# Performance work log

Measured on AMD Instinct MI355X. Metric: run time of the kernel, lower is better.

The kernel has to match this reference:

```python
import jax, jax.numpy as jnp
import numpy as np

HIDDEN = 2048
NUM_HEADS = 16
NUM_KV_HEADS = 4
HEAD_DIM = HIDDEN // NUM_HEADS  # 128
ROPE_THETA = 1000000.0
B, S = 2, 2048


def setup_inputs() -> dict:
    key = jax.random.key(0)
    ks = jax.random.split(key, 10)
    sc = 0.02
    return {
        "hidden_states": jax.random.normal(ks[0], (B, S, HIDDEN), jnp.float32),
        "position_ids": jnp.broadcast_to(jnp.arange(S, dtype=jnp.int32), (B, S)),
        "Wq": jax.random.normal(ks[1], (HIDDEN, NUM_HEADS * HEAD_DIM), jnp.float32) * sc,
        "bq": jnp.zeros((NUM_HEADS * HEAD_DIM,), jnp.float32),
        "Wk": jax.random.normal(ks[2], (HIDDEN, NUM_KV_HEADS * HEAD_DIM), jnp.float32) * sc,
        "bk": jnp.zeros((NUM_KV_HEADS * HEAD_DIM,), jnp.float32),
        "Wv": jax.random.normal(ks[3], (HIDDEN, NUM_KV_HEADS * HEAD_DIM), jnp.float32) * sc,
        "bv": jnp.zeros((NUM_KV_HEADS * HEAD_DIM,), jnp.float32),
        "Wo": jax.random.normal(ks[4], (NUM_HEADS * HEAD_DIM, HIDDEN), jnp.float32) * sc,
        "bo": jnp.zeros((HIDDEN,), jnp.float32),
    }


def _rope_cos_sin(position_ids, dtype):
    # inv_freq: [head_dim/2]
    inv_freq = 1.0 / (ROPE_THETA ** (jnp.arange(0, HEAD_DIM, 2, dtype=jnp.float32) / HEAD_DIM))
    freqs = position_ids.astype(jnp.float32)[:, :, None] * inv_freq[None, None, :]  # [B,S,d/2]
    emb = jnp.concatenate([freqs, freqs], axis=-1)  # [B,S,d]
    return jnp.cos(emb).astype(dtype), jnp.sin(emb).astype(dtype)


def _rotate_half(x):
    h = x.shape[-1] // 2
    return jnp.concatenate([-x[..., h:], x[..., :h]], axis=-1)


def _attention(hidden_states, position_ids, Wq, bq, Wk, bk, Wv, bv, Wo, bo):
    bsz, q_len, _ = hidden_states.shape
    q = (hidden_states @ Wq + bq).reshape(bsz, q_len, NUM_HEADS, HEAD_DIM).transpose(0, 2, 1, 3)
    k = (hidden_states @ Wk + bk).reshape(bsz, q_len, NUM_KV_HEADS, HEAD_DIM).transpose(0, 2, 1, 3)
    v = (hidden_states @ Wv + bv).reshape(bsz, q_len, NUM_KV_HEADS, HEAD_DIM).transpose(0, 2, 1, 3)

    cos, sin = _rope_cos_sin(position_ids, hidden_states.dtype)
    cos = cos[:, None, :, :]  # [B,1,S,d]
    sin = sin[:, None, :, :]
    q = q * cos + _rotate_half(q) * sin
    k = k * cos + _rotate_half(k) * sin

    # repeat_kv (GQA): [B,kvh,S,d] -> [B,H,S,d]
    n_rep = NUM_HEADS // NUM_KV_HEADS
    k = jnp.repeat(k, n_rep, axis=1)
    v = jnp.repeat(v, n_rep, axis=1)

    scale = 1.0 / jnp.sqrt(jnp.array(HEAD_DIM, hidden_states.dtype))
    scores = jnp.einsum('bhqd,bhkd->bhqk', q, k) * scale  # [B,H,S,S]
    causal = jnp.tril(jnp.ones((q_len, q_len), bool))
    scores = jnp.where(causal[None, None], scores, jnp.finfo(scores.dtype).min)
    probs = jax.nn.softmax(scores.astype(jnp.float32), axis=-1).astype(hidden_states.dtype)
    attn = jnp.einsum('bhqk,bhkd->bhqd', probs, v)
    attn = attn.transpose(0, 2, 1, 3).reshape(bsz, q_len, HIDDEN)
    return attn @ Wo + bo


def reference(hidden_states, position_ids, Wq, bq, Wk, bk, Wv, bv, Wo, bo):
    return _attention(hidden_states, position_ids, Wq, bq, Wk, bk, Wv, bv, Wo, bo)
```

## Files before the change

### kernel.cpp

```cpp
#include <hip/hip_runtime.h>
#include <cmath>

#define HIDDEN 2048
#define NH 16
#define NKV 4
#define HD 128
#define SEQ 2048
#define BATCH 2

typedef unsigned short ushort_t;
typedef short bf16x8 __attribute__((ext_vector_type(8)));
typedef float f32x4 __attribute__((ext_vector_type(4)));
typedef ushort_t u16x4 __attribute__((ext_vector_type(4)));

__device__ __forceinline__ ushort_t f2bf(float f) {
    union { float f; unsigned int u; } v; v.f = f;
    unsigned int r = v.u + 0x7fffu + ((v.u >> 16) & 1u);
    return (ushort_t)(r >> 16);
}
__device__ __forceinline__ ushort_t f2bf_trunc(float f) {
    union { float f; unsigned int u; } v; v.f = f;
    return (ushort_t)(v.u >> 16);
}

__device__ __forceinline__ f32x4 mfma16(bf16x8 a, bf16x8 b, f32x4 c) {
    return __builtin_amdgcn_mfma_f32_16x16x32_bf16(a, b, c, 0, 0, 0);
}

__device__ __forceinline__ void load_lds16(const void* g, void* l) {
    __builtin_amdgcn_global_load_lds((const __attribute__((address_space(1))) unsigned int*)g,
                                     (__attribute__((address_space(3))) unsigned int*)l,
                                     16, 0, 0);
}


__global__ __launch_bounds__(256) void convert_x(const float* __restrict__ x,
                                                 ushort_t* __restrict__ xb, int n4) {
    int g = blockIdx.x * 256 + threadIdx.x;
    if (g >= n4) return;
    float4 v = ((const float4*)x)[g];
    u16x4 o;
    o[0] = f2bf(v.x); o[1] = f2bf(v.y); o[2] = f2bf(v.z); o[3] = f2bf(v.w);
    ((u16x4*)xb)[g] = o;
}

__global__ __launch_bounds__(256) void transpose_all(const float* __restrict__ Wq,
                                                     const float* __restrict__ Wk,
                                                     const float* __restrict__ Wv,
                                                     const float* __restrict__ Wo,
                                                     ushort_t* __restrict__ WqkvT,
                                                     ushort_t* __restrict__ WoT) {
    const int z = blockIdx.z;
    const float* W;
    ushort_t* WT;
    int N;
    if (z == 0)      { W = Wq; WT = WqkvT;                        N = 2048; }
    else if (z == 1) { W = Wk; WT = WqkvT + 2048ull * 2048;       N = 512;  }
    else if (z == 2) { W = Wv; WT = WqkvT + 2560ull * 2048;       N = 512;  }
    else             { W = Wo; WT = WoT;                          N = 2048; }
    const int K = 2048;
    const int n0 = blockIdx.x * 64, k0 = blockIdx.y * 64;
    if (n0 >= N) return;
    __shared__ ushort_t T[64][72];
    const int t = threadIdx.x;
    for (int idx = t; idx < 64 * 16; idx += 256) {
        int r = idx >> 4, c4 = (idx & 15) << 2;
        float4 v = *(const float4*)&W[(size_t)(k0 + r) * N + n0 + c4];
        T[r][c4 + 0] = f2bf(v.x); T[r][c4 + 1] = f2bf(v.y);
        T[r][c4 + 2] = f2bf(v.z); T[r][c4 + 3] = f2bf(v.w);
    }
    __syncthreads();
    for (int idx = t; idx < 64 * 16; idx += 256) {
        int n = idx >> 4, kg = (idx & 15) << 2;
        u16x4 o;
        o[0] = T[kg + 0][n]; o[1] = T[kg + 1][n];
        o[2] = T[kg + 2][n]; o[3] = T[kg + 3][n];
        *(u16x4*)&WT[(size_t)(n0 + n) * K + k0 + kg] = o;
    }
}

template <int MODE, int BK>
__global__ __launch_bounds__(256) void gemm_bt(const ushort_t* __restrict__ A,
                                               const ushort_t* __restrict__ Bt,
                                               const float* __restrict__ bias,
                                               const float* __restrict__ bias2,
                                               const float* __restrict__ bias3,
                                               void* __restrict__ out,
                                               void* __restrict__ out2,
                                               void* __restrict__ out3,
                                               int M, int N, int K,
                                               const int* __restrict__ posids) {
    constexpr int CH = BK / 32;
    __shared__ __align__(16) ushort_t As[2 * CH * 4096];
    __shared__ __align__(16) ushort_t Bs[2 * CH * 4096];
    const int tid = threadIdx.x;
    const int w = tid >> 6, lane = tid & 63, quad = lane >> 4, l16 = lane & 15;
    const int wr = w >> 1, wc = w & 1;
    const int m0 = blockIdx.y * 128, n0 = blockIdx.x * 128;

    f32x4 acc[4][4];
    for (int i = 0; i < 4; i++)
        for (int j = 0; j < 4; j++)
            for (int e = 0; e < 4; e++) acc[i][j][e] = 0.0f;

    const int rr = lane >> 2;
    const int gc8 = (((lane & 3) ^ ((lane >> 3) & 3)) << 3);
    const ushort_t* Ag = A + (size_t)(m0 + w * 32 + rr) * K + gc8;
    const ushort_t* Bg = Bt + (size_t)(n0 + w * 32 + rr) * K + gc8;
    ushort_t* Asw = As + w * 1024;
    ushort_t* Bsw = Bs + w * 1024;

    auto stage = [&](int bi, int k0) {
#pragma unroll
        for (int kc = 0; kc < CH; kc++) {
            const ushort_t* ag = Ag + k0 + kc * 32;
            const ushort_t* bg = Bg + k0 + kc * 32;
            ushort_t* la = Asw + (bi * CH + kc) * 4096;
            ushort_t* lb = Bsw + (bi * CH + kc) * 4096;
            load_lds16(ag, la);
            load_lds16(ag + (size_t)16 * K, la + 512);
            load_lds16(bg, lb);
            load_lds16(bg + (size_t)16 * K, lb + 512);
        }
    };

    const int nk = K / BK;
    const int rsw = ((l16 >> 1) & 3);
    stage(0, 0);
    __syncthreads();

    for (int ki = 0; ki < nk; ki++) {
        const int cur = ki & 1;
        if (ki + 1 < nk) stage(cur ^ 1, (ki + 1) * BK);
#pragma unroll
        for (int kc = 0; kc < CH; kc++) {
            const ushort_t* Ab = &As[(cur * CH + kc) * 4096];
            const ushort_t* Bb = &Bs[(cur * CH + kc) * 4096];
            bf16x8 af[4];
#pragma unroll
            for (int i = 0; i < 4; i++)
                af[i] = *(const bf16x8*)&Ab[(wr * 64 + i * 16 + l16) * 32 + ((quad ^ rsw) << 3)];
#pragma unroll
            for (int j = 0; j < 4; j++) {
                bf16x8 bf = *(const bf16x8*)&Bb[((wc + 2 * j) * 16 + l16) * 32 +
                                                ((quad ^ rsw) << 3)];
#pragma unroll
                for (int i = 0; i < 4; i++) acc[i][j] = mfma16(af[i], bf, acc[i][j]);
            }
        }
        __syncthreads();
    }

    if (MODE == 0) {
        float* O = (float*)out;
#pragma unroll
        for (int i = 0; i < 4; i++)
#pragma unroll
            for (int r = 0; r < 4; r++) {
                int row = m0 + wr * 64 + i * 16 + quad * 4 + r;
#pragma unroll
                for (int j = 0; j < 4; j++) {
                    int col = n0 + (wc + 2 * j) * 16 + l16;
                    O[(size_t)row * N + col] = acc[i][j][r] + bias[col];
                }
            }
    } else {
        if (n0 < 2048) {
            ushort_t* O = (ushort_t*)out;
            const int h = n0 >> 7;
            const float scale = 0.08838834764831845f;
            float fr[2];
#pragma unroll
            for (int p = 0; p < 2; p++)
                fr[p] = __expf(-0.21586735246819178f * (float)((wc + 2 * p) * 16 + l16));
#pragma unroll
            for (int i = 0; i < 4; i++)
#pragma unroll
                for (int r = 0; r < 4; r++) {
                    int row = m0 + wr * 64 + i * 16 + quad * 4 + r;
                    int b = row >> 11, s = row & (SEQ - 1);
                    float pos = (float)posids[row];
                    size_t obase = ((size_t)(b * NH + h) * SEQ + s) * HD;
#pragma unroll
                    for (int p = 0; p < 2; p++) {
                        int dl = (wc + 2 * p) * 16 + l16;
                        float x1 = acc[i][p][r] + bias[n0 + dl];
                        float x2 = acc[i][p + 2][r] + bias[n0 + dl + 64];
                        float sn, cs;
                        __sincosf(pos * fr[p], &sn, &cs);
                        O[obase + dl]      = f2bf((x1 * cs - x2 * sn) * scale);
                        O[obase + dl + 64] = f2bf((x2 * cs + x1 * sn) * scale);
                    }
                }
        } else if (n0 < 2560) {
            ushort_t* O = (ushort_t*)out2;
            const int n0k = n0 - 2048;
            const int h = n0k >> 7;
            float fr[2];
#pragma unroll
            for (int p = 0; p < 2; p++)
                fr[p] = __expf(-0.21586735246819178f * (float)((wc + 2 * p) * 16 + l16));
#pragma unroll
            for (int i = 0; i < 4; i++)
#pragma unroll
                for (int r = 0; r < 4; r++) {
                    int row = m0 + wr * 64 + i * 16 + quad * 4 + r;
                    int b = row >> 11, s = row & (SEQ - 1);
                    float pos = (float)posids[row];
                    size_t obase = ((size_t)(b * NKV + h) * SEQ + s) * HD;
#pragma unroll
                    for (int p = 0; p < 2; p++) {
                        int dl = (wc + 2 * p) * 16 + l16;
                        float x1 = acc[i][p][r] + bias2[n0k + dl];
                        float x2 = acc[i][p + 2][r] + bias2[n0k + dl + 64];
                        float sn, cs;
                        __sincosf(pos * fr[p], &sn, &cs);
                        O[obase + dl]      = f2bf(x1 * cs - x2 * sn);
                        O[obase + dl + 64] = f2bf(x2 * cs + x1 * sn);
                    }
                }
        } else {
            ushort_t* O = (ushort_t*)out3;
            const int n0v = n0 - 2560;
            const int h = n0v >> 7;
#pragma unroll
            for (int i = 0; i < 4; i++)
#pragma unroll
                for (int r = 0; r < 4; r++) {
                    int row = m0 + wr * 64 + i * 16 + quad * 4 + r;
                    int b = row >> 11, s = row & (SEQ - 1);
#pragma unroll
                    for (int j = 0; j < 4; j++) {
                        int d = (wc + 2 * j) * 16 + l16;
                        float v = acc[i][j][r] + bias3[n0v + d];
                        O[((size_t)(b * NKV + h) * HD + d) * SEQ + s] = f2bf(v);
                    }
                }
        }
    }
}

__global__ __launch_bounds__(256) void flash(const ushort_t* __restrict__ Qr,
                                             const ushort_t* __restrict__ Kr,
                                             const ushort_t* __restrict__ Vt,
                                             ushort_t* __restrict__ Attn) {
    __shared__ __align__(16) ushort_t Ksh[2 * 4 * 64 * 32];
    __shared__ __align__(16) ushort_t Vsh[2 * 2 * 128 * 32];
    __shared__ __align__(16) ushort_t Ps[4 * 16 * 72];
    const int tid = threadIdx.x;
    const int w = tid >> 6, lane = tid & 63, quad = lane >> 4, l16 = lane & 15;
    const int x = blockIdx.x, h = blockIdx.y, b = blockIdx.z;
    const int qt = b ? x : (gridDim.x - 1 - x);
    const int q0 = qt * 128;
    const int nkt = 2 * qt + 2;
    const int hkv = h >> 2;
    const ushort_t* Kg = Kr + ((size_t)(b * NKV + hkv) * SEQ) * HD;
    const ushort_t* Vg = Vt + ((size_t)(b * NKV + hkv) * HD) * SEQ;

    const int p = lane >> 2;
    const int gc8 = (((lane & 3) ^ ((lane >> 3) & 3)) << 3);
    const ushort_t* kst = Kg + (size_t)p * HD + w * 32 + gc8;
    const ushort_t* vst = Vg + (size_t)((w & 1) * 64 + p) * SEQ + (w >> 1) * 32 + gc8;
    ushort_t* ksl = Ksh + w * 2048;
    ushort_t* vsl = Vsh + (w >> 1) * 4096 + (w & 1) * 2048;

    auto stage = [&](int bi, int kv0) {
        const ushort_t* gk = kst + (size_t)kv0 * HD;
        ushort_t* lk = ksl + bi * 8192;
        load_lds16(gk, lk);
        load_lds16(gk + (size_t)16 * HD, lk + 512);
        load_lds16(gk + (size_t)32 * HD, lk + 1024);
        load_lds16(gk + (size_t)48 * HD, lk + 1536);
        const ushort_t* gv = vst + kv0;
        ushort_t* lv = vsl + bi * 8192;
        load_lds16(gv, lv);
        load_lds16(gv + (size_t)16 * SEQ, lv + 512);
        load_lds16(gv + (size_t)32 * SEQ, lv + 1024);
        load_lds16(gv + (size_t)48 * SEQ, lv + 1536);
    };

    bf16x8 aq[2][4];
#pragma unroll
    for (int st = 0; st < 2; st++) {
        const size_t qrow = ((size_t)(b * NH + h) * SEQ + q0 + st * 64 + w * 16 + l16) * HD;
#pragma unroll
        for (int kc = 0; kc < 4; kc++)
            aq[st][kc] = *(const bf16x8*)&Qr[qrow + kc * 32 + quad * 8];
    }

    f32x4 o[2][8];
#pragma unroll
    for (int st = 0; st < 2; st++)
#pragma unroll
        for (int j = 0; j < 8; j++)
#pragma unroll
            for (int e = 0; e < 4; e++) o[st][j][e] = 0.0f;
    f32x4 ls2[2];
#pragma unroll
    for (int st = 0; st < 2; st++)
        for (int e = 0; e < 4; e++) ls2[st][e] = 0.0f;
    bf16x8 ones;
#pragma unroll
    for (int e = 0; e < 8; e++) ones[e] = (short)0x3F80;

    ushort_t* Pw = &Ps[w * 16 * 72];
    const int rsw8 = ((l16 >> 1) & 3) << 3;

    stage(0, 0);
    __syncthreads();

    for (int kt = 0; kt < nkt; kt++) {
        const int kv0 = kt * 64;
        const int cur = kt & 1;
        if (kt + 1 < nkt) stage(cur ^ 1, kv0 + 64);

        const ushort_t* Kb = Ksh + cur * 8192;
        const ushort_t* Vb = Vsh + cur * 8192;

#pragma unroll
        for (int st = 0; st < 2; st++) {
            if (st == 0 && kt == 2 * qt + 1) continue;

            f32x4 sa[4];
#pragma unroll
            for (int nt = 0; nt < 4; nt++)
#pragma unroll
                for (int e = 0; e < 4; e++) sa[nt][e] = 0.0f;
#pragma unroll
            for (int kc = 0; kc < 4; kc++) {
#pragma unroll
                for (int nt = 0; nt < 4; nt++) {
                    bf16x8 bk = *(const bf16x8*)&Kb[kc * 2048 + nt * 512 + l16 * 32 +
                                                    ((quad * 8) ^ rsw8)];
                    sa[nt] = mfma16(aq[st][kc], bk, sa[nt]);
                }
            }

            if ((kt >> 1) == qt && (kt & 1) == st) {
#pragma unroll
                for (int nt = 0; nt < 4; nt++)
#pragma unroll
                    for (int r = 0; r < 4; r++) {
                        int kvg = kv0 + nt * 16 + l16;
                        int qg = q0 + st * 64 + w * 16 + quad * 4 + r;
                        if (kvg > qg) sa[nt][r] = -1e30f;
                    }
            }

#pragma unroll
            for (int nt = 0; nt < 4; nt++)
#pragma unroll
                for (int r = 0; r < 4; r++)
                    Pw[(quad * 4 + r) * 72 + nt * 16 + l16] = f2bf_trunc(__expf(sa[nt][r]));

#pragma unroll
            for (int kc = 0; kc < 2; kc++) {
                bf16x8 ap = *(const bf16x8*)&Pw[l16 * 72 + kc * 32 + quad * 8];
                ls2[st] = mfma16(ap, ones, ls2[st]);
#pragma unroll
                for (int j = 0; j < 8; j++) {
                    bf16x8 bv = *(const bf16x8*)&Vb[kc * 4096 + (j * 16 + l16) * 32 +
                                                    ((quad * 8) ^ rsw8)];
                    o[st][j] = mfma16(ap, bv, o[st][j]);
                }
            }
        }
        __syncthreads();
    }

#pragma unroll
    for (int st = 0; st < 2; st++)
#pragma unroll
        for (int r = 0; r < 4; r++) {
            float inv = 1.0f / ls2[st][r];
            int row = b * SEQ + q0 + st * 64 + w * 16 + quad * 4 + r;
            size_t obase = (size_t)row * HIDDEN + h * HD;
#pragma unroll
            for (int j = 0; j < 8; j++) Attn[obase + j * 16 + l16] = f2bf(o[st][j][r] * inv);
        }
}

extern "C" void kernel_launch(void* const* d_in, const int* in_sizes, int n_in,
                              void* d_out, int out_size, void* d_ws, size_t ws_size,
                              hipStream_t stream) {
    const float* hs = (const float*)d_in[0];
    const int* posids = (const int*)d_in[1];
    const float* Wq = (const float*)d_in[2];
    const float* bq = (const float*)d_in[3];
    const float* Wk = (const float*)d_in[4];
    const float* bk = (const float*)d_in[5];
    const float* Wv = (const float*)d_in[6];
    const float* bv = (const float*)d_in[7];
    const float* Wo = (const float*)d_in[8];
    const float* bo = (const float*)d_in[9];
    float* out = (float*)d_out;

    char* ws = (char*)d_ws;
    size_t off = 0;
    auto alloc = [&](size_t bytes) {
        char* p = ws + off;
        off += (bytes + 255) & ~(size_t)255;
        return p;
    };
    ushort_t* Xb     = (ushort_t*)alloc(4096ull * 2048 * 2);
    ushort_t* WqkvT  = (ushort_t*)alloc(3072ull * 2048 * 2);
    ushort_t* WoT    = (ushort_t*)alloc(2048ull * 2048 * 2);
    ushort_t* Qr     = (ushort_t*)alloc((size_t)BATCH * NH * SEQ * HD * 2);
    ushort_t* Kr     = (ushort_t*)alloc((size_t)BATCH * NKV * SEQ * HD * 2);
    ushort_t* Vtr    = (ushort_t*)alloc((size_t)BATCH * NKV * HD * SEQ * 2);
    ushort_t* Attn   = (ushort_t*)alloc(4096ull * 2048 * 2);

    convert_x<<<4096 * 2048 / 4 / 256, 256, 0, stream>>>(hs, Xb, 4096 * 2048 / 4);
    transpose_all<<<dim3(32, 32, 4), 256, 0, stream>>>(Wq, Wk, Wv, Wo, WqkvT, WoT);

    gemm_bt<2, 32><<<dim3(24, 32), 256, 0, stream>>>(Xb, WqkvT, bq, bk, bv,
                                                     Qr, Kr, Vtr, 4096, 3072, 2048, posids);

    flash<<<dim3(SEQ / 128, NH, BATCH), 256, 0, stream>>>(Qr, Kr, Vtr, Attn);

    gemm_bt<0, 64><<<dim3(16, 32), 256, 0, stream>>>(Attn, WoT, bo, nullptr, nullptr,
                                                     out, nullptr, nullptr, 4096, 2048, 2048, nullptr);
}
```

Measured before the change: 354.9 us.

## Replace 128x128 GEMMs with 256x256 tile, 512-thread, triple-buffered pipeline

Both projection GEMMs now use a 256x256 output tile with 8 waves, a 3-stage LDS ring, explicit vmcnt waits, raw barriers and raised scheduling priority around the MFMA block. The goal is more operand reuse per LDS load and deeper overlap of global loads with compute. The RoPE and V-transpose epilogues are remapped to the new column layout. The trade-off is that the grid shrinks to 192 and 128 blocks on 256 CUs, which underfills the device, and register and LDS pressure rise.

Measured after the change: 365.2 us. 1.03x slower.

```diff
diff --git a/kernel.cpp b/kernel.cpp
--- a/kernel.cpp
+++ b/kernel.cpp
@@ -79,8 +79,8 @@
     }
 }
 
-template <int MODE, int BK>
-__global__ __launch_bounds__(256) void gemm_bt(const ushort_t* __restrict__ A,
+template <int MODE>
+__global__ __launch_bounds__(512) void gemm256(const ushort_t* __restrict__ A,
                                                const ushort_t* __restrict__ Bt,
                                                const float* __restrict__ bias,
                                                const float* __restrict__ bias2,
@@ -90,104 +90,121 @@
                                                void* __restrict__ out3,
                                                int M, int N, int K,
                                                const int* __restrict__ posids) {
-    constexpr int CH = BK / 32;
-    __shared__ __align__(16) ushort_t As[2 * CH * 4096];
-    __shared__ __align__(16) ushort_t Bs[2 * CH * 4096];
+    __shared__ __align__(16) ushort_t Asb[3 * 8192];
+    __shared__ __align__(16) ushort_t Bsb[3 * 8192];
     const int tid = threadIdx.x;
     const int w = tid >> 6, lane = tid & 63, quad = lane >> 4, l16 = lane & 15;
-    const int wr = w >> 1, wc = w & 1;
-    const int m0 = blockIdx.y * 128, n0 = blockIdx.x * 128;
-
-    f32x4 acc[4][4];
-    for (int i = 0; i < 4; i++)
+    const int wr = w >> 2, wc = w & 3;
+    const int m0 = blockIdx.y * 256, n0 = blockIdx.x * 256;
+
+    f32x4 acc[8][4];
+#pragma unroll
+    for (int i = 0; i < 8; i++)
+#pragma unroll
         for (int j = 0; j < 4; j++)
+#pragma unroll
             for (int e = 0; e < 4; e++) acc[i][j][e] = 0.0f;
 
-    const int rr = lane >> 2;
-    const int gc8 = (((lane & 3) ^ ((lane >> 3) & 3)) << 3);
-    const ushort_t* Ag = A + (size_t)(m0 + w * 32 + rr) * K + gc8;
-    const ushort_t* Bg = Bt + (size_t)(n0 + w * 32 + rr) * K + gc8;
-    ushort_t* Asw = As + w * 1024;
-    ushort_t* Bsw = Bs + w * 1024;
-
-    auto stage = [&](int bi, int k0) {
-#pragma unroll
-        for (int kc = 0; kc < CH; kc++) {
-            const ushort_t* ag = Ag + k0 + kc * 32;
-            const ushort_t* bg = Bg + k0 + kc * 32;
-            ushort_t* la = Asw + (bi * CH + kc) * 4096;
-            ushort_t* lb = Bsw + (bi * CH + kc) * 4096;
-            load_lds16(ag, la);
-            load_lds16(ag + (size_t)16 * K, la + 512);
-            load_lds16(bg, lb);
-            load_lds16(bg + (size_t)16 * K, lb + 512);
-        }
+    const int lr = tid >> 2;
+    const int c8 = (((lane & 3) ^ ((lane >> 3) & 3)) << 3);
+    const ushort_t* Ag = A + (size_t)(m0 + lr) * K + c8;
+    const ushort_t* Bg = Bt + (size_t)(n0 + lr) * K + c8;
+    ushort_t* Alw = Asb + w * 512;
+    ushort_t* Blw = Bsb + w * 512;
+
+    auto stage = [&](int t, int buf) {
+        const int k0 = t * 32;
+        const ushort_t* ag = Ag + k0;
+        const ushort_t* bg = Bg + k0;
+        ushort_t* la = Alw + buf * 8192;
+        ushort_t* lb = Blw + buf * 8192;
+        load_lds16(ag, la);
+        load_lds16(ag + (size_t)128 * K, la + 4096);
+        load_lds16(bg, lb);
+        load_lds16(bg + (size_t)128 * K, lb + 4096);
     };
 
-    const int nk = K / BK;
-    const int rsw = ((l16 >> 1) & 3);
+    const int rsw = (l16 >> 1) & 3;
+    const int aoff = (wr * 128 + l16) * 32 + ((quad ^ rsw) << 3);
+    const int boff = (wc * 16 + l16) * 32 + ((quad ^ rsw) << 3);
+
+    auto compute = [&](int buf) {
+        const ushort_t* Ab = Asb + buf * 8192 + aoff;
+        const ushort_t* Bb = Bsb + buf * 8192 + boff;
+        bf16x8 bfr[4], af[8];
+#pragma unroll
+        for (int j = 0; j < 4; j++) bfr[j] = *(const bf16x8*)&Bb[j * 2048];
+#pragma unroll
+        for (int i = 0; i < 8; i++) af[i] = *(const bf16x8*)&Ab[i * 512];
+        __builtin_amdgcn_s_setprio(1);
+#pragma unroll
+        for (int i = 0; i < 8; i++)
+#pragma unroll
+            for (int j = 0; j < 4; j++) acc[i][j] = mfma16(af[i], bfr[j], acc[i][j]);
+        __builtin_amdgcn_s_setprio(0);
+    };
+
+    const int nt = K >> 5;
     stage(0, 0);
-    __syncthreads();
-
-    for (int ki = 0; ki < nk; ki++) {
-        const int cur = ki & 1;
-        if (ki + 1 < nk) stage(cur ^ 1, (ki + 1) * BK);
-#pragma unroll
-        for (int kc = 0; kc < CH; kc++) {
-            const ushort_t* Ab = &As[(cur * CH + kc) * 4096];
-            const ushort_t* Bb = &Bs[(cur * CH + kc) * 4096];
-            bf16x8 af[4];
-#pragma unroll
-            for (int i = 0; i < 4; i++)
-                af[i] = *(const bf16x8*)&Ab[(wr * 64 + i * 16 + l16) * 32 + ((quad ^ rsw) << 3)];
-#pragma unroll
-            for (int j = 0; j < 4; j++) {
-                bf16x8 bf = *(const bf16x8*)&Bb[((wc + 2 * j) * 16 + l16) * 32 +
-                                                ((quad ^ rsw) << 3)];
-#pragma unroll
-                for (int i = 0; i < 4; i++) acc[i][j] = mfma16(af[i], bf, acc[i][j]);
-            }
-        }
-        __syncthreads();
-    }
+    stage(1, 1);
+    int cur = 0, nx = 2;
+    for (int t = 0; t < nt - 2; ++t) {
+        stage(t + 2, nx);
+        asm volatile("s_waitcnt vmcnt(8)" ::: "memory");
+        __builtin_amdgcn_s_barrier();
+        __builtin_amdgcn_sched_barrier(0);
+        compute(cur);
+        __builtin_amdgcn_sched_barrier(0);
+        __builtin_amdgcn_s_barrier();
+        cur = (cur == 2) ? 0 : cur + 1;
+        nx = (nx == 2) ? 0 : nx + 1;
+    }
+    asm volatile("s_waitcnt vmcnt(4)" ::: "memory");
+    __builtin_amdgcn_s_barrier();
+    __builtin_amdgcn_sched_barrier(0);
+    compute(cur);
+    __builtin_amdgcn_sched_barrier(0);
+    __builtin_amdgcn_s_barrier();
+    cur = (cur == 2) ? 0 : cur + 1;
+    asm volatile("s_waitcnt vmcnt(0)" ::: "memory");
+    __builtin_amdgcn_s_barrier();
+    __builtin_amdgcn_sched_barrier(0);
+    compute(cur);
 
     if (MODE == 0) {
         float* O = (float*)out;
 #pragma unroll
-        for (int i = 0; i < 4; i++)
+        for (int i = 0; i < 8; i++)
 #pragma unroll
             for (int r = 0; r < 4; r++) {
-                int row = m0 + wr * 64 + i * 16 + quad * 4 + r;
+                int row = m0 + wr * 128 + i * 16 + quad * 4 + r;
 #pragma unroll
                 for (int j = 0; j < 4; j++) {
-                    int col = n0 + (wc + 2 * j) * 16 + l16;
+                    int col = n0 + (wc + 4 * j) * 16 + l16;
                     O[(size_t)row * N + col] = acc[i][j][r] + bias[col];
                 }
             }
     } else {
         if (n0 < 2048) {
             ushort_t* O = (ushort_t*)out;
-            const int h = n0 >> 7;
+            const int h0 = n0 >> 7;
             const float scale = 0.08838834764831845f;
-            float fr[2];
-#pragma unroll
-            for (int p = 0; p < 2; p++)
-                fr[p] = __expf(-0.21586735246819178f * (float)((wc + 2 * p) * 16 + l16));
-#pragma unroll
-            for (int i = 0; i < 4; i++)
+            const int dl = wc * 16 + l16;
+            const float fr = __expf(-0.21586735246819178f * (float)dl);
+#pragma unroll
+            for (int i = 0; i < 8; i++)
 #pragma unroll
                 for (int r = 0; r < 4; r++) {
-                    int row = m0 + wr * 64 + i * 16 + quad * 4 + r;
+                    int row = m0 + wr * 128 + i * 16 + quad * 4 + r;
                     int b = row >> 11, s = row & (SEQ - 1);
                     float pos = (float)posids[row];
-                    size_t obase = ((size_t)(b * NH + h) * SEQ + s) * HD;
+                    float sn, cs;
+                    __sincosf(pos * fr, &sn, &cs);
 #pragma unroll
                     for (int p = 0; p < 2; p++) {
-                        int dl = (wc + 2 * p) * 16 + l16;
-                        float x1 = acc[i][p][r] + bias[n0 + dl];
-                        float x2 = acc[i][p + 2][r] + bias[n0 + dl + 64];
-                        float sn, cs;
-                        __sincosf(pos * fr[p], &sn, &cs);
+                        float x1 = acc[i][2 * p][r] + bias[n0 + p * 128 + dl];
+                        float x2 = acc[i][2 * p + 1][r] + bias[n0 + p * 128 + dl + 64];
+                        size_t obase = ((size_t)(b * NH + h0 + p) * SEQ + s) * HD;
                         O[obase + dl]      = f2bf((x1 * cs - x2 * sn) * scale);
                         O[obase + dl + 64] = f2bf((x2 * cs + x1 * sn) * scale);
                     }
@@ -195,26 +212,23 @@
         } else if (n0 < 2560) {
             ushort_t* O = (ushort_t*)out2;
             const int n0k = n0 - 2048;
-            const int h = n0k >> 7;
-            float fr[2];
-#pragma unroll
-            for (int p = 0; p < 2; p++)
-                fr[p] = __expf(-0.21586735246819178f * (float)((wc + 2 * p) * 16 + l16));
-#pragma unroll
-            for (int i = 0; i < 4; i++)
+            const int h0 = n0k >> 7;
+            const int dl = wc * 16 + l16;
+            const float fr = __expf(-0.21586735246819178f * (float)dl);
+#pragma unroll
+            for (int i = 0; i < 8; i++)
 #pragma unroll
                 for (int r = 0; r < 4; r++) {
-                    int row = m0 + wr * 64 + i * 16 + quad * 4 + r;
+                    int row = m0 + wr * 128 + i * 16 + quad * 4 + r;
                     int b = row >> 11, s = row & (SEQ - 1);
                     float pos = (float)posids[row];
-                    size_t obase = ((size_t)(b * NKV + h) * SEQ + s) * HD;
+                    float sn, cs;
+                    __sincosf(pos * fr, &sn, &cs);
 #pragma unroll
                     for (int p = 0; p < 2; p++) {
-                        int dl = (wc + 2 * p) * 16 + l16;
-                        float x1 = acc[i][p][r] + bias2[n0k + dl];
-                        float x2 = acc[i][p + 2][r] + bias2[n0k + dl + 64];
-                        float sn, cs;
-                        __sincosf(pos * fr[p], &sn, &cs);
+                        float x1 = acc[i][2 * p][r] + bias2[n0k + p * 128 + dl];
+                        float x2 = acc[i][2 * p + 1][r] + bias2[n0k + p * 128 + dl + 64];
+                        size_t obase = ((size_t)(b * NKV + h0 + p) * SEQ + s) * HD;
                         O[obase + dl]      = f2bf(x1 * cs - x2 * sn);
                         O[obase + dl + 64] = f2bf(x2 * cs + x1 * sn);
                     }
@@ -222,17 +236,18 @@
         } else {
             ushort_t* O = (ushort_t*)out3;
             const int n0v = n0 - 2560;
-            const int h = n0v >> 7;
-#pragma unroll
-            for (int i = 0; i < 4; i++)
+#pragma unroll
+            for (int i = 0; i < 8; i++)
 #pragma unroll
                 for (int r = 0; r < 4; r++) {
-                    int row = m0 + wr * 64 + i * 16 + quad * 4 + r;
+                    int row = m0 + wr * 128 + i * 16 + quad * 4 + r;
                     int b = row >> 11, s = row & (SEQ - 1);
 #pragma unroll
                     for (int j = 0; j < 4; j++) {
-                        int d = (wc + 2 * j) * 16 + l16;
-                        float v = acc[i][j][r] + bias3[n0v + d];
+                        int ct = wc + 4 * j;
+                        int h = (n0v >> 7) + (ct >> 3);
+                        int d = (ct & 7) * 16 + l16;
+                        float v = acc[i][j][r] + bias3[n0v + ct * 16 + l16];
                         O[((size_t)(b * NKV + h) * HD + d) * SEQ + s] = f2bf(v);
                     }
                 }
@@ -413,11 +428,11 @@
     convert_x<<<4096 * 2048 / 4 / 256, 256, 0, stream>>>(hs, Xb, 4096 * 2048 / 4);
     transpose_all<<<dim3(32, 32, 4), 256, 0, stream>>>(Wq, Wk, Wv, Wo, WqkvT, WoT);
 
-    gemm_bt<2, 32><<<dim3(24, 32), 256, 0, stream>>>(Xb, WqkvT, bq, bk, bv,
-                                                     Qr, Kr, Vtr, 4096, 3072, 2048, posids);
+    gemm256<2><<<dim3(12, 16), 512, 0, stream>>>(Xb, WqkvT, bq, bk, bv,
+                                                 Qr, Kr, Vtr, 4096, 3072, 2048, posids);
 
     flash<<<dim3(SEQ / 128, NH, BATCH), 256, 0, stream>>>(Qr, Kr, Vtr, Attn);
 
-    gemm_bt<0, 64><<<dim3(16, 32), 256, 0, stream>>>(Attn, WoT, bo, nullptr, nullptr,
-                                                     out, nullptr, nullptr, 4096, 2048, 2048, nullptr);
-}
+    gemm256<0><<<dim3(8, 16), 512, 0, stream>>>(Attn, WoT, bo, nullptr, nullptr,
+                                                out, nullptr, nullptr, 4096, 2048, 2048, nullptr);
+}
```

## Triple-buffer GEMM pipeline with vmcnt waits; read V directly from global in flash

Applied to the files above, without the earlier changes.

The GEMM kernel moves from double buffering with full syncthreads to a three-stage LDS ring. It uses explicit s_waitcnt vmcnt, raw barriers, sched_barrier fences and setprio around the MFMA block, so two tiles' loads stay in flight while one computes. BK is fixed at 32 for both projections, which removes the BK=64 variant used for the output projection. The flash kernel drops the V LDS staging and reads V fragments straight from global memory in the PV loop. That saves LDS and load instructions but exposes global latency and uncoalesced strided reads inside the inner loop.

Result: slower. 437.6 us (+23.3%).

```diff
diff --git a/kernel.cpp b/kernel.cpp
--- a/kernel.cpp
+++ b/kernel.cpp
@@ -79,8 +79,8 @@
     }
 }
 
-template <int MODE, int BK>
-__global__ __launch_bounds__(256) void gemm_bt(const ushort_t* __restrict__ A,
+template <int MODE>
+__global__ __launch_bounds__(256) void gemm128(const ushort_t* __restrict__ A,
                                                const ushort_t* __restrict__ Bt,
                                                const float* __restrict__ bias,
                                                const float* __restrict__ bias2,
@@ -90,66 +90,86 @@
                                                void* __restrict__ out3,
                                                int M, int N, int K,
                                                const int* __restrict__ posids) {
-    constexpr int CH = BK / 32;
-    __shared__ __align__(16) ushort_t As[2 * CH * 4096];
-    __shared__ __align__(16) ushort_t Bs[2 * CH * 4096];
+    __shared__ __align__(16) ushort_t Asb[3 * 4096];
+    __shared__ __align__(16) ushort_t Bsb[3 * 4096];
     const int tid = threadIdx.x;
     const int w = tid >> 6, lane = tid & 63, quad = lane >> 4, l16 = lane & 15;
     const int wr = w >> 1, wc = w & 1;
     const int m0 = blockIdx.y * 128, n0 = blockIdx.x * 128;
 
     f32x4 acc[4][4];
+#pragma unroll
     for (int i = 0; i < 4; i++)
+#pragma unroll
         for (int j = 0; j < 4; j++)
+#pragma unroll
             for (int e = 0; e < 4; e++) acc[i][j][e] = 0.0f;
 
     const int rr = lane >> 2;
     const int gc8 = (((lane & 3) ^ ((lane >> 3) & 3)) << 3);
     const ushort_t* Ag = A + (size_t)(m0 + w * 32 + rr) * K + gc8;
     const ushort_t* Bg = Bt + (size_t)(n0 + w * 32 + rr) * K + gc8;
-    ushort_t* Asw = As + w * 1024;
-    ushort_t* Bsw = Bs + w * 1024;
-
-    auto stage = [&](int bi, int k0) {
-#pragma unroll
-        for (int kc = 0; kc < CH; kc++) {
-            const ushort_t* ag = Ag + k0 + kc * 32;
-            const ushort_t* bg = Bg + k0 + kc * 32;
-            ushort_t* la = Asw + (bi * CH + kc) * 4096;
-            ushort_t* lb = Bsw + (bi * CH + kc) * 4096;
-            load_lds16(ag, la);
-            load_lds16(ag + (size_t)16 * K, la + 512);
-            load_lds16(bg, lb);
-            load_lds16(bg + (size_t)16 * K, lb + 512);
-        }
+    ushort_t* Asw = Asb + w * 1024;
+    ushort_t* Bsw = Bsb + w * 1024;
+
+    auto stage = [&](int t, int buf) {
+        const int k0 = t * 32;
+        const ushort_t* ag = Ag + k0;
+        const ushort_t* bg = Bg + k0;
+        ushort_t* la = Asw + buf * 4096;
+        ushort_t* lb = Bsw + buf * 4096;
+        load_lds16(ag, la);
+        load_lds16(ag + (size_t)16 * K, la + 512);
+        load_lds16(bg, lb);
+        load_lds16(bg + (size_t)16 * K, lb + 512);
     };
 
-    const int nk = K / BK;
-    const int rsw = ((l16 >> 1) & 3);
+    const int rsw = (l16 >> 1) & 3;
+    const int aoff = (wr * 64 + l16) * 32 + ((quad ^ rsw) << 3);
+    const int boff = (wc * 16 + l16) * 32 + ((quad ^ rsw) << 3);
+
+    auto compute = [&](int buf) {
+        const ushort_t* Ab = Asb + buf * 4096 + aoff;
+        const ushort_t* Bb = Bsb + buf * 4096 + boff;
+        bf16x8 af[4], bfr[4];
+#pragma unroll
+        for (int i = 0; i < 4; i++) af[i] = *(const bf16x8*)&Ab[i * 512];
+#pragma unroll
+        for (int j = 0; j < 4; j++) bfr[j] = *(const bf16x8*)&Bb[j * 1024];
+        __builtin_amdgcn_s_setprio(1);
+#pragma unroll
+        for (int i = 0; i < 4; i++)
+#pragma unroll
+            for (int j = 0; j < 4; j++) acc[i][j] = mfma16(af[i], bfr[j], acc[i][j]);
+        __builtin_amdgcn_s_setprio(0);
+    };
+
+    const int nt = K >> 5;
     stage(0, 0);
-    __syncthreads();
-
-    for (int ki = 0; ki < nk; ki++) {
-        const int cur = ki & 1;
-        if (ki + 1 < nk) stage(cur ^ 1, (ki + 1) * BK);
-#pragma unroll
-        for (int kc = 0; kc < CH; kc++) {
-            const ushort_t* Ab = &As[(cur * CH + kc) * 4096];
-            const ushort_t* Bb = &Bs[(cur * CH + kc) * 4096];
-            bf16x8 af[4];
-#pragma unroll
-            for (int i = 0; i < 4; i++)
-                af[i] = *(const bf16x8*)&Ab[(wr * 64 + i * 16 + l16) * 32 + ((quad ^ rsw) << 3)];
-#pragma unroll
-            for (int j = 0; j < 4; j++) {
-                bf16x8 bf = *(const bf16x8*)&Bb[((wc + 2 * j) * 16 + l16) * 32 +
-                                                ((quad ^ rsw) << 3)];
-#pragma unroll
-                for (int i = 0; i < 4; i++) acc[i][j] = mfma16(af[i], bf, acc[i][j]);
-            }
-        }
-        __syncthreads();
-    }
+    stage(1, 1);
+    int cur = 0, nx = 2;
+    for (int t = 0; t < nt - 2; ++t) {
+        stage(t + 2, nx);
+        asm volatile("s_waitcnt vmcnt(8)" ::: "memory");
+        __builtin_amdgcn_s_barrier();
+        __builtin_amdgcn_sched_barrier(0);
+        compute(cur);
+        __builtin_amdgcn_sched_barrier(0);
+        __builtin_amdgcn_s_barrier();
+        cur = (cur == 2) ? 0 : cur + 1;
+        nx = (nx == 2) ? 0 : nx + 1;
+    }
+    asm volatile("s_waitcnt vmcnt(4)" ::: "memory");
+    __builtin_amdgcn_s_barrier();
+    __builtin_amdgcn_sched_barrier(0);
+    compute(cur);
+    __builtin_amdgcn_sched_barrier(0);
+    __builtin_amdgcn_s_barrier();
+    cur = (cur == 2) ? 0 : cur + 1;
+    asm volatile("s_waitcnt vmcnt(0)" ::: "memory");
+    __builtin_amdgcn_s_barrier();
+    __builtin_amdgcn_sched_barrier(0);
+    compute(cur);
 
     if (MODE == 0) {
         float* O = (float*)out;
@@ -245,7 +265,6 @@
                                              const ushort_t* __restrict__ Vt,
                                              ushort_t* __restrict__ Attn) {
     __shared__ __align__(16) ushort_t Ksh[2 * 4 * 64 * 32];
-    __shared__ __align__(16) ushort_t Vsh[2 * 2 * 128 * 32];
     __shared__ __align__(16) ushort_t Ps[4 * 16 * 72];
     const int tid = threadIdx.x;
     const int w = tid >> 6, lane = tid & 63, quad = lane >> 4, l16 = lane & 15;
@@ -260,9 +279,7 @@
     const int p = lane >> 2;
     const int gc8 = (((lane & 3) ^ ((lane >> 3) & 3)) << 3);
     const ushort_t* kst = Kg + (size_t)p * HD + w * 32 + gc8;
-    const ushort_t* vst = Vg + (size_t)((w & 1) * 64 + p) * SEQ + (w >> 1) * 32 + gc8;
     ushort_t* ksl = Ksh + w * 2048;
-    ushort_t* vsl = Vsh + (w >> 1) * 4096 + (w & 1) * 2048;
 
     auto stage = [&](int bi, int kv0) {
         const ushort_t* gk = kst + (size_t)kv0 * HD;
@@ -271,12 +288,6 @@
         load_lds16(gk + (size_t)16 * HD, lk + 512);
         load_lds16(gk + (size_t)32 * HD, lk + 1024);
         load_lds16(gk + (size_t)48 * HD, lk + 1536);
-        const ushort_t* gv = vst + kv0;
-        ushort_t* lv = vsl + bi * 8192;
-        load_lds16(gv, lv);
-        load_lds16(gv + (size_t)16 * SEQ, lv + 512);
-        load_lds16(gv + (size_t)32 * SEQ, lv + 1024);
-        load_lds16(gv + (size_t)48 * SEQ, lv + 1536);
     };
 
     bf16x8 aq[2][4];
@@ -315,7 +326,6 @@
         if (kt + 1 < nkt) stage(cur ^ 1, kv0 + 64);
 
         const ushort_t* Kb = Ksh + cur * 8192;
-        const ushort_t* Vb = Vsh + cur * 8192;
 
 #pragma unroll
         for (int st = 0; st < 2; st++) {
@@ -359,8 +369,8 @@
                 ls2[st] = mfma16(ap, ones, ls2[st]);
 #pragma unroll
                 for (int j = 0; j < 8; j++) {
-                    bf16x8 bv = *(const bf16x8*)&Vb[kc * 4096 + (j * 16 + l16) * 32 +
-                                                    ((quad * 8) ^ rsw8)];
+                    bf16x8 bv = *(const bf16x8*)&Vg[(size_t)(j * 16 + l16) * SEQ +
+                                                    kv0 + kc * 32 + quad * 8];
                     o[st][j] = mfma16(ap, bv, o[st][j]);
                 }
             }
@@ -413,11 +423,11 @@
     convert_x<<<4096 * 2048 / 4 / 256, 256, 0, stream>>>(hs, Xb, 4096 * 2048 / 4);
     transpose_all<<<dim3(32, 32, 4), 256, 0, stream>>>(Wq, Wk, Wv, Wo, WqkvT, WoT);
 
-    gemm_bt<2, 32><<<dim3(24, 32), 256, 0, stream>>>(Xb, WqkvT, bq, bk, bv,
-                                                     Qr, Kr, Vtr, 4096, 3072, 2048, posids);
+    gemm128<2><<<dim3(24, 32), 256, 0, stream>>>(Xb, WqkvT, bq, bk, bv,
+                                                 Qr, Kr, Vtr, 4096, 3072, 2048, posids);
 
     flash<<<dim3(SEQ / 128, NH, BATCH), 256, 0, stream>>>(Qr, Kr, Vtr, Attn);
 
-    gemm_bt<0, 64><<<dim3(16, 32), 256, 0, stream>>>(Attn, WoT, bo, nullptr, nullptr,
-                                                     out, nullptr, nullptr, 4096, 2048, 2048, nullptr);
-}
+    gemm128<0><<<dim3(16, 32), 256, 0, stream>>>(Attn, WoT, bo, nullptr, nullptr,
+                                                 out, nullptr, nullptr, 4096, 2048, 2048, nullptr);
+}
```
